# Kernel optimization log

Hardware: AMD Instinct MI355X
Metric: run time of the kernel (lower is better)

## Reference

```python
import jax, jax.numpy as jnp
import numpy as np

K = 16  # nsample for knn_point

def _bn(x, g, b):
    # inference-mode BatchNorm1d folded to per-channel affine (running stats 0/1)
    return x * g[None, :, None] + b[None, :, None]

def _knn(xyz, k):
    # xyz: [B,3,N] -> idx [B,N,k] of k nearest neighbors (squared L2)
    p = xyz.transpose(0, 2, 1)                                   # [B,N,3]
    sq = jnp.sum(p * p, axis=-1)                                 # [B,N]
    d = sq[:, :, None] + sq[:, None, :] - 2.0 * jnp.einsum('bnc,bmc->bnm', p, p)
    _, idx = jax.lax.top_k(-d, k)
    return idx

def _gather(hT, idx):
    # hT: [B,N,C], idx: [B,N,K] -> [B,N,K,C]
    return jax.vmap(lambda a, i: a[i])(hT, idx)

def setup_inputs():
    key = jax.random.key(0)
    ks = jax.random.split(key, 12)
    B, N, C = 16, 2048, 128
    def w(k, shape, fan):
        return jax.random.normal(k, shape, jnp.float32) * (1.0 / np.sqrt(fan))
    o = jnp.ones; z = jnp.zeros
    return {
        'points': jax.random.normal(ks[0], (B, 6, N), jnp.float32),
        'label': jax.random.uniform(ks[1], (B, 1, 16), jnp.float32),
        'We1': w(ks[2], (C, 6), 6), 'ge1': o(C), 'be1': z(C),
        'We2': w(ks[3], (C, C), C), 'ge2': o(C), 'be2': z(C),
        'W1': w(ks[4], (3, C, C), C), 'g1': o((3, C)), 'b1': z((3, C)),
        'W2': w(ks[5], (3, C, C), C), 'g2': o((3, C)), 'b2': z((3, C)),
        'Wf': w(ks[6], (1024, 3 * C), 3 * C), 'gf': o(1024), 'bf': z(1024),
        'Wl': w(ks[7], (64, 16), 16), 'gl': o(64), 'bl': z(64),
        'Wc1': w(ks[8], (512, 3136), 3136), 'bc1': z(512), 'gc1': o(512), 'bb1': z(512),
        'Wc2': w(ks[9], (256, 512), 512), 'bc2': z(256), 'gc2': o(256), 'bb2': z(256),
        'Wc3': w(ks[10], (50, 256), 256), 'bc3': z(50),
    }

def reference(points, label, We1, ge1, be1, We2, ge2, be2, W1, g1, b1, W2, g2, b2,
              Wf, gf, bf, Wl, gl, bl, Wc1, bc1, gc1, bb1, Wc2, bc2, gc2, bb2, Wc3, bc3):
    B, _, N = points.shape
    x = points[:, :6, :]
    xyz = x[:, :3, :]
    idx = _knn(xyz, K)                                            # [B,N,16]
    # input embedding: two conv1x1 + BN + ReLU
    h = jax.nn.relu(_bn(jnp.einsum('oc,bcn->bon', We1, x), ge1, be1))
    h = jax.nn.relu(_bn(jnp.einsum('oc,bcn->bon', We2, h), ge2, be2))
    xs = []
    for i in range(3):  # PVDSA_Res blocks (simplified: conv-BN-ReLU, kNN max-agg, conv-BN + residual)
        t = jax.nn.relu(_bn(jnp.einsum('oc,bcn->bon', W1[i], h), g1[i], b1[i]))
        nbr = _gather(t.transpose(0, 2, 1), idx)                  # [B,N,K,C]
        m = nbr.max(axis=2).transpose(0, 2, 1)                    # [B,C,N]
        h = jax.nn.relu(_bn(jnp.einsum('oc,bcn->bon', W2[i], m), g2[i], b2[i]) + h)
        xs.append(h)
    xcat = jnp.concatenate(xs, axis=1)                            # [B,384,N]
    xf = jax.nn.leaky_relu(_bn(jnp.einsum('oc,bcn->bon', Wf, xcat), gf, bf), 0.2)  # [B,1024,N]
    x_max = xf.max(axis=-1)                                       # [B,1024]
    x_avg = xf.mean(axis=-1)                                      # [B,1024]
    cls = jnp.broadcast_to(label.transpose(0, 2, 1), (B, 16, N))
    lab = jax.nn.leaky_relu(_bn(jnp.einsum('oc,bcn->bon', Wl, cls), gl, bl), 0.2)  # [B,64,N]
    glob = jnp.concatenate([
        jnp.broadcast_to(x_max[:, :, None], (B, 1024, N)),
        jnp.broadcast_to(x_avg[:, :, None], (B, 1024, N)),
        lab], axis=1)
    xa = jnp.concatenate([xf, glob], axis=1)                      # [B,3136,N]
    c = jax.nn.relu(_bn(jnp.einsum('oc,bcn->bon', Wc1, xa) + bc1[None, :, None], gc1, bb1))
    c = jax.nn.relu(_bn(jnp.einsum('oc,bcn->bon', Wc2, c) + bc2[None, :, None], gc2, bb2))
    out = jnp.einsum('oc,bcn->bon', Wc3, c) + bc3[None, :, None]  # [B,50,N]
    return out
```

## Files before the change

### kernel.cpp

```cpp
#include <hip/hip_runtime.h>
#include <cstdint>
#include <cstddef>

#define DEVINL __device__ __forceinline__

typedef float    f32x4 __attribute__((ext_vector_type(4)));
typedef _Float16 f16x8 __attribute__((ext_vector_type(8)));
typedef _Float16 f16x4 __attribute__((ext_vector_type(4)));

constexpr int BB = 16, NN = 2048, MM = 32768;

constexpr size_t OFF_WE1 = 0;
constexpr size_t OFF_WE2 = OFF_WE1 + 128 * 64 * 2;
constexpr size_t OFF_W1  = OFF_WE2 + 128 * 128 * 2;
constexpr size_t OFF_W2  = OFF_W1  + 3 * 128 * 128 * 2;
constexpr size_t OFF_WF  = OFF_W2  + 3 * 128 * 128 * 2;
constexpr size_t OFF_WC1 = OFF_WF  + 1024 * 384 * 2;
constexpr size_t OFF_WC2 = OFF_WC1 + 512 * 1024 * 2;
constexpr size_t OFF_WC3 = OFF_WC2 + 256 * 512 * 2;
constexpr size_t OFF_BC2 = OFF_WC3 + 128 * 256 * 2;
constexpr size_t OFF_BC3 = OFF_BC2 + 256 * 4;
constexpr size_t OFF_CVEC= OFF_BC3 + 128 * 4;
constexpr size_t OFF_PMAX= OFF_CVEC+ 16 * 512 * 4;
constexpr size_t OFF_PSUM= OFF_PMAX+ 16 * 16 * 1024 * 4;
constexpr size_t OFF_IDX = OFF_PSUM+ 16 * 16 * 1024 * 4;
constexpr size_t OFF_R1  = 8ull << 20;
constexpr size_t OFF_X0  = OFF_R1;
constexpr size_t OFF_HT  = OFF_R1 + (4ull  << 20);
constexpr size_t OFF_TT  = OFF_R1 + (12ull << 20);
constexpr size_t OFF_MT  = OFF_R1 + (20ull << 20);
constexpr size_t OFF_C1  = OFF_R1;
constexpr size_t OFF_XCAT= OFF_R1 + (32ull << 20);
constexpr size_t OFF_C2  = OFF_XCAT;
constexpr size_t OFF_XF  = OFF_XCAT + (24ull << 20);

__global__ __launch_bounds__(256) void fold_all_kernel(
    const float* We1, const float* ge1, const float* We2, const float* ge2,
    const float* W1,  const float* g1,  const float* W2,  const float* g2,
    const float* Wf,  const float* gf,  const float* Wc1, const float* gc1,
    const float* Wc2, const float* gc2, const float* Wc3,
    const float* gc2b, const float* bc2, const float* bb2, const float* bc3,
    const float* pts, char* ws)
{
    const int bid = blockIdx.x;
    const int tid = threadIdx.x;

    if (bid == 4704) {
        ((float*)(ws + OFF_BC2))[tid] = gc2b[tid] * bc2[tid] + bb2[tid];
        return;
    }
    if (bid == 4705) {
        if (tid < 128) ((float*)(ws + OFF_BC3))[tid] = (tid < 50) ? bc3[tid] : 0.f;
        return;
    }
    if (bid >= 4706) {
        int m = (bid - 4706) * 256 + tid;
        int b = m >> 11, n = m & 2047;
        const float* ps = pts + (size_t)b * 6 * 2048 + n;
        _Float16 tmp[64];
#pragma unroll
        for (int c = 0; c < 64; ++c) tmp[c] = (_Float16)0.f;
#pragma unroll
        for (int c = 0; c < 6; ++c) tmp[c] = (_Float16)ps[(size_t)c << 11];
        _Float16* dst = (_Float16*)(ws + OFF_X0) + (size_t)m * 64;
#pragma unroll
        for (int v = 0; v < 8; ++v) *(f16x8*)(dst + v * 8) = *(const f16x8*)(tmp + v * 8);
        return;
    }

    int id, base;
    if      (bid < 32)   { id = 0;  base = 0;    }
    else if (bid < 96)   { id = 1;  base = 32;   }
    else if (bid < 160)  { id = 2;  base = 96;   }
    else if (bid < 224)  { id = 3;  base = 160;  }
    else if (bid < 288)  { id = 4;  base = 224;  }
    else if (bid < 352)  { id = 5;  base = 288;  }
    else if (bid < 416)  { id = 6;  base = 352;  }
    else if (bid < 480)  { id = 7;  base = 416;  }
    else if (bid < 2016) { id = 8;  base = 480;  }
    else if (bid < 4064) { id = 9;  base = 2016; }
    else if (bid < 4576) { id = 10; base = 4064; }
    else                 { id = 11; base = 4576; }

    const float* src = nullptr; const float* g = nullptr; _Float16* dst = nullptr;
    int O = 0, K = 0, lds = 0, Kp = 0;
    switch (id) {
        case 0:  src = We1; g = ge1; O = 128; K = 6;    lds = 6;    Kp = 64;   dst = (_Float16*)(ws + OFF_WE1); break;
        case 1:  src = We2; g = ge2; O = 128; K = 128;  lds = 128;  Kp = 128;  dst = (_Float16*)(ws + OFF_WE2); break;
        case 2: case 3: case 4: {
            int i = id - 2;
            src = W1 + (size_t)i * 16384; g = g1 + i * 128; O = 128; K = 128; lds = 128; Kp = 128;
            dst = (_Float16*)(ws + OFF_W1) + (size_t)i * 16384; break; }
        case 5: case 6: case 7: {
            int i = id - 5;
            src = W2 + (size_t)i * 16384; g = g2 + i * 128; O = 128; K = 128; lds = 128; Kp = 128;
            dst = (_Float16*)(ws + OFF_W2) + (size_t)i * 16384; break; }
        case 8:  src = Wf;  g = gf;  O = 1024; K = 384;  lds = 384;  Kp = 384;  dst = (_Float16*)(ws + OFF_WF);  break;
        case 9:  src = Wc1; g = gc1; O = 512;  K = 1024; lds = 3136; Kp = 1024; dst = (_Float16*)(ws + OFF_WC1); break;
        case 10: src = Wc2; g = gc2; O = 256;  K = 512;  lds = 512;  Kp = 512;  dst = (_Float16*)(ws + OFF_WC2); break;
        default: src = Wc3; g = nullptr; O = 50; K = 256; lds = 256; Kp = 256;  dst = (_Float16*)(ws + OFF_WC3); break;
    }
    int e = (bid - base) * 256 + tid;
    int o = e / Kp, k = e - o * Kp;
    float v = 0.f;
    if (o < O && k < K) {
        v = src[(size_t)o * lds + k];
        if (g) v *= g[o];
    }
    dst[e] = (_Float16)v;
}

DEVINL float knn_dist(const float4 pq, const float4 pm) {
    float t = pq.x * pm.x;
    t = fmaf(pq.y, pm.y, t);
    t = fmaf(pq.z, pm.z, t);
    return fmaf(-2.f, t, pm.w);
}

#define KNN_DINS(X) do { \
    const float x_ = (X); \
    d15 = __builtin_amdgcn_fmed3f(x_, d14, d15); \
    d14 = __builtin_amdgcn_fmed3f(x_, d13, d14); \
    d13 = __builtin_amdgcn_fmed3f(x_, d12, d13); \
    d12 = __builtin_amdgcn_fmed3f(x_, d11, d12); \
    d11 = __builtin_amdgcn_fmed3f(x_, d10, d11); \
    d10 = __builtin_amdgcn_fmed3f(x_, d9,  d10); \
    d9  = __builtin_amdgcn_fmed3f(x_, d8,  d9);  \
    d8  = __builtin_amdgcn_fmed3f(x_, d7,  d8);  \
    d7  = __builtin_amdgcn_fmed3f(x_, d6,  d7);  \
    d6  = __builtin_amdgcn_fmed3f(x_, d5,  d6);  \
    d5  = __builtin_amdgcn_fmed3f(x_, d4,  d5);  \
    d4  = __builtin_amdgcn_fmed3f(x_, d3,  d4);  \
    d3  = __builtin_amdgcn_fmed3f(x_, d2,  d3);  \
    d2  = __builtin_amdgcn_fmed3f(x_, d1,  d2);  \
    d1  = __builtin_amdgcn_fmed3f(x_, d0,  d1);  \
    d0  = __builtin_amdgcn_fmed3f(x_, -3.4e38f, d0); \
} while (0)

#define KNN_CE(A, B) { const float lo_ = fminf(A, B), hi_ = fmaxf(A, B); A = lo_; B = hi_; }

#define KNN_MERGE(OFF) do { \
    const float n0  = __shfl_xor(d0,  OFF), n1  = __shfl_xor(d1,  OFF), \
                n2  = __shfl_xor(d2,  OFF), n3  = __shfl_xor(d3,  OFF), \
                n4  = __shfl_xor(d4,  OFF), n5  = __shfl_xor(d5,  OFF), \
                n6  = __shfl_xor(d6,  OFF), n7  = __shfl_xor(d7,  OFF), \
                n8  = __shfl_xor(d8,  OFF), n9  = __shfl_xor(d9,  OFF), \
                n10 = __shfl_xor(d10, OFF), n11 = __shfl_xor(d11, OFF), \
                n12 = __shfl_xor(d12, OFF), n13 = __shfl_xor(d13, OFF), \
                n14 = __shfl_xor(d14, OFF), n15 = __shfl_xor(d15, OFF); \
    d0  = fminf(d0,  n15); d1  = fminf(d1,  n14); d2  = fminf(d2,  n13); d3  = fminf(d3,  n12); \
    d4  = fminf(d4,  n11); d5  = fminf(d5,  n10); d6  = fminf(d6,  n9);  d7  = fminf(d7,  n8);  \
    d8  = fminf(d8,  n7);  d9  = fminf(d9,  n6);  d10 = fminf(d10, n5);  d11 = fminf(d11, n4);  \
    d12 = fminf(d12, n3);  d13 = fminf(d13, n2);  d14 = fminf(d14, n1);  d15 = fminf(d15, n0);  \
    KNN_CE(d0, d8)  KNN_CE(d1, d9)  KNN_CE(d2, d10) KNN_CE(d3, d11) \
    KNN_CE(d4, d12) KNN_CE(d5, d13) KNN_CE(d6, d14) KNN_CE(d7, d15) \
    KNN_CE(d0, d4)  KNN_CE(d1, d5)  KNN_CE(d2, d6)  KNN_CE(d3, d7)  \
    KNN_CE(d8, d12) KNN_CE(d9, d13) KNN_CE(d10,d14) KNN_CE(d11,d15) \
    KNN_CE(d0, d2)  KNN_CE(d1, d3)  KNN_CE(d4, d6)  KNN_CE(d5, d7)  \
    KNN_CE(d8, d10) KNN_CE(d9, d11) KNN_CE(d12,d14) KNN_CE(d13,d15) \
    KNN_CE(d0, d1)  KNN_CE(d2, d3)  KNN_CE(d4, d5)  KNN_CE(d6, d7)  \
    KNN_CE(d8, d9)  KNN_CE(d10,d11) KNN_CE(d12,d13) KNN_CE(d14,d15) \
// ... 89 lines not shown
    _Float16* B2s = SH + 28672;

    const int tid = threadIdx.x;
    const int lane = tid & 63, wave = tid >> 6;
    const int r = lane & 15, quad = lane >> 4;
    const int m_blk = blockIdx.x * 64;
    const int oh = (wave >> 1) * 64, mh = (wave & 1) * 32;

    const int srow  = wave * 8 + (lane >> 3);
    const int sslot = lane & 7;

#pragma unroll
    for (int t = 0; t < 4; ++t) {
        const int row = t * 32 + srow;
        const int gk = (sslot ^ (row & 7)) << 3;
        __builtin_amdgcn_global_load_lds(
            (const __attribute__((address_space(1))) unsigned int*)(W1e + (size_t)row * 64 + gk),
            (__attribute__((address_space(3))) unsigned int*)(A1s + t * 2048 + wave * 512),
            16, 0, 0);
    }
#pragma unroll
    for (int t = 0; t < 2; ++t) {
        const int row = t * 32 + srow;
        const int gk = (sslot ^ (row & 7)) << 3;
        __builtin_amdgcn_global_load_lds(
            (const __attribute__((address_space(1))) unsigned int*)(X + (size_t)(m_blk + row) * 64 + gk),
            (__attribute__((address_space(3))) unsigned int*)(B1s + t * 2048 + wave * 512),
            16, 0, 0);
    }
#pragma unroll
    for (int kt = 0; kt < 2; ++kt)
#pragma unroll
        for (int t = 0; t < 4; ++t) {
            const int row = t * 32 + srow;
            const int gk = kt * 64 + ((sslot ^ (row & 7)) << 3);
            __builtin_amdgcn_global_load_lds(
                (const __attribute__((address_space(1))) unsigned int*)(W2e + (size_t)row * 128 + gk),
                (__attribute__((address_space(3))) unsigned int*)(A2s + kt * 8192 + t * 2048 + wave * 512),
                16, 0, 0);
        }

    asm volatile("s_waitcnt vmcnt(8)" ::: "memory");
    __builtin_amdgcn_sched_barrier(0);
    __builtin_amdgcn_s_barrier();
    asm volatile("" ::: "memory");

    f32x4 acc1[4][2];
#pragma unroll
    for (int a = 0; a < 4; ++a)
#pragma unroll
        for (int c = 0; c < 2; ++c) acc1[a][c] = (f32x4){0.f, 0.f, 0.f, 0.f};
#pragma unroll
    for (int ks = 0; ks < 2; ++ks) {
        f16x8 af[4], bf[2];
#pragma unroll
        for (int oi = 0; oi < 4; ++oi) {
            const int row = oh + oi * 16 + r;
            const int slot = (ks * 4 + quad) ^ (row & 7);
            af[oi] = *(const f16x8*)(A1s + row * 64 + slot * 8);
        }
#pragma unroll
        for (int mi = 0; mi < 2; ++mi) {
            const int row = mh + mi * 16 + r;
            const int slot = (ks * 4 + quad) ^ (row & 7);
            bf[mi] = *(const f16x8*)(B1s + row * 64 + slot * 8);
        }
#pragma unroll
        for (int oi = 0; oi < 4; ++oi)
#pragma unroll
            for (int mi = 0; mi < 2; ++mi)
                acc1[oi][mi] = __builtin_amdgcn_mfma_f32_16x16x32_f16(af[oi], bf[mi], acc1[oi][mi], 0, 0, 0);
    }

#pragma unroll
    for (int oi = 0; oi < 4; ++oi) {
        const int ob = oh + oi * 16 + quad * 4;
        const f32x4 bv = *(const f32x4*)(b1v + ob);
        const int kt = ob >> 6, kk = ob & 63;
        const int chunk = kk >> 3, within = kk & 7;
#pragma unroll
        for (int mi = 0; mi < 2; ++mi) {
            const int row = mh + mi * 16 + r;
            f32x4 v = acc1[oi][mi] + bv;
            f16x4 ov;
#pragma unroll
            for (int j = 0; j < 4; ++j) { float x = v[j]; ov[j] = (_Float16)((x > 0.f) ? x : 0.f); }
            *(f16x4*)(B2s + kt * 4096 + row * 64 + ((chunk ^ (row & 7)) << 3) + within) = ov;
        }
    }
    __syncthreads();

    f32x4 acc2[4][2];
#pragma unroll
    for (int a = 0; a < 4; ++a)
#pragma unroll
        for (int c = 0; c < 2; ++c) acc2[a][c] = (f32x4){0.f, 0.f, 0.f, 0.f};
#pragma unroll
    for (int kt = 0; kt < 2; ++kt)
#pragma unroll
        for (int ks = 0; ks < 2; ++ks) {
            f16x8 af[4], bf[2];
#pragma unroll
            for (int oi = 0; oi < 4; ++oi) {
                const int row = oh + oi * 16 + r;
                const int slot = (ks * 4 + quad) ^ (row & 7);
                af[oi] = *(const f16x8*)(A2s + kt * 8192 + row * 64 + slot * 8);
            }
#pragma unroll
            for (int mi = 0; mi < 2; ++mi) {
                const int row = mh + mi * 16 + r;
                const int slot = (ks * 4 + quad) ^ (row & 7);
                bf[mi] = *(const f16x8*)(B2s + kt * 4096 + row * 64 + slot * 8);
            }
#pragma unroll
            for (int oi = 0; oi < 4; ++oi)
#pragma unroll
                for (int mi = 0; mi < 2; ++mi)
                    acc2[oi][mi] = __builtin_amdgcn_mfma_f32_16x16x32_f16(af[oi], bf[mi], acc2[oi][mi], 0, 0, 0);
        }
    __syncthreads();

    _Float16* OT = SH;
#pragma unroll
    for (int oi = 0; oi < 4; ++oi) {
        const int ol = oh + oi * 16 + quad * 4;
        const f32x4 bv = *(const f32x4*)(b2v + ol);
#pragma unroll
        for (int mi = 0; mi < 2; ++mi) {
            const int row = mh + mi * 16 + r;
            f32x4 v = acc2[oi][mi] + bv;
            f16x4 ov;
#pragma unroll
            for (int j = 0; j < 4; ++j) { float x = v[j]; ov[j] = (_Float16)((x > 0.f) ? x : 0.f); }
            const int s = ((ol >> 2) ^ (row & 31)) << 2;
            *(f16x4*)(OT + row * 128 + s) = ov;
        }
    }
    __syncthreads();
#pragma unroll
    for (int it2 = 0; it2 < 4; ++it2) {
        const int row = it2 * 16 + (tid >> 4);
        const int c = tid & 15;
        const int s0 = ((c * 2) ^ (row & 31)) << 2;
        const int s1 = ((c * 2 + 1) ^ (row & 31)) << 2;
        f16x4 a  = *(const f16x4*)(OT + row * 128 + s0);
        f16x4 b2 = *(const f16x4*)(OT + row * 128 + s1);
        f16x8 o8;
        o8[0] = a[0]; o8[1] = a[1]; o8[2] = a[2]; o8[3] = a[3];
        o8[4] = b2[0]; o8[5] = b2[1]; o8[6] = b2[2]; o8[7] = b2[3];
        *(f16x8*)(Y + (size_t)(m_blk + row) * 128 + c * 8) = o8;
    }
}

__global__ __launch_bounds__(256) void pair_kernel(
    const _Float16* __restrict__ Wa, const _Float16* __restrict__ Wb,
    const _Float16* __restrict__ X, const _Float16* __restrict__ Res,
    _Float16* __restrict__ Y1, _Float16* __restrict__ Y2,
    const float* __restrict__ ba, const float* __restrict__ bb,
    int ldR, int roff, int yoff1)
{
    __shared__ _Float16 SH[32768];
    _Float16* Aa  = SH;
    _Float16* Bx  = SH + 16384;
    _Float16* By1 = SH + 24576;
    _Float16* Ab  = SH;
    _Float16* OT2 = SH + 16384;

    const int tid = threadIdx.x;
    const int lane = tid & 63, wave = tid >> 6;
    const int r = lane & 15, quad = lane >> 4;
    const int m_blk = blockIdx.x * 64;
    const int oh = (wave >> 1) * 64, mh = (wave & 1) * 32;

    const int srow  = wave * 8 + (lane >> 3);
    const int sslot = lane & 7;

#pragma unroll
    for (int kt = 0; kt < 2; ++kt)
#pragma unroll
        for (int t = 0; t < 4; ++t) {
            const int row = t * 32 + srow;
            const int gk = kt * 64 + ((sslot ^ (row & 7)) << 3);
            __builtin_amdgcn_global_load_lds(
                (const __attribute__((address_space(1))) unsigned int*)(Wa + (size_t)row * 128 + gk),
                (__attribute__((address_space(3))) unsigned int*)(Aa + kt * 8192 + t * 2048 + wave * 512),
                16, 0, 0);
        }
#pragma unroll
    for (int kt = 0; kt < 2; ++kt)
#pragma unroll
        for (int t = 0; t < 2; ++t) {
            const int row = t * 32 + srow;
            const int gk = kt * 64 + ((sslot ^ (row & 7)) << 3);
            __builtin_amdgcn_global_load_lds(
                (const __attribute__((address_space(1))) unsigned int*)(X + (size_t)(m_blk + row) * 128 + gk),
                (__attribute__((address_space(3))) unsigned int*)(Bx + kt * 4096 + t * 2048 + wave * 512),
                16, 0, 0);
        }
    __syncthreads();

    f32x4 acc1[4][2];
#pragma unroll
    for (int a = 0; a < 4; ++a)
#pragma unroll
        for (int c = 0; c < 2; ++c) acc1[a][c] = (f32x4){0.f, 0.f, 0.f, 0.f};
#pragma unroll
    for (int kt = 0; kt < 2; ++kt)
#pragma unroll
        for (int ks = 0; ks < 2; ++ks) {
            f16x8 af[4], bf[2];
#pragma unroll
            for (int oi = 0; oi < 4; ++oi) {
                const int row = oh + oi * 16 + r;
                const int slot = (ks * 4 + quad) ^ (row & 7);
                af[oi] = *(const f16x8*)(Aa + kt * 8192 + row * 64 + slot * 8);
            }
#pragma unroll
            for (int mi = 0; mi < 2; ++mi) {
                const int row = mh + mi * 16 + r;
                const int slot = (ks * 4 + quad) ^ (row & 7);
                bf[mi] = *(const f16x8*)(Bx + kt * 4096 + row * 64 + slot * 8);
            }
#pragma unroll
            for (int oi = 0; oi < 4; ++oi)
#pragma unroll
                for (int mi = 0; mi < 2; ++mi)
                    acc1[oi][mi] = __builtin_amdgcn_mfma_f32_16x16x32_f16(af[oi], bf[mi], acc1[oi][mi], 0, 0, 0);
        }
    __syncthreads();

#pragma unroll
    for (int kt = 0; kt < 2; ++kt)
#pragma unroll
        for (int t = 0; t < 4; ++t) {
            const int row = t * 32 + srow;
            const int gk = kt * 64 + ((sslot ^ (row & 7)) << 3);
            __builtin_amdgcn_global_load_lds(
                (const __attribute__((address_space(1))) unsigned int*)(Wb + (size_t)row * 128 + gk),
                (__attribute__((address_space(3))) unsigned int*)(Ab + kt * 8192 + t * 2048 + wave * 512),
                16, 0, 0);
        }

#pragma unroll
    for (int oi = 0; oi < 4; ++oi) {
        const int ol = oh + oi * 16 + quad * 4;
        const f32x4 bv = *(const f32x4*)(ba + ol);
        const int kt = ol >> 6, kk = ol & 63;
        const int chunk = kk >> 3, within = kk & 7;
#pragma unroll
        for (int mi = 0; mi < 2; ++mi) {
            const int row = mh + mi * 16 + r;
            f32x4 v = acc1[oi][mi] + bv;
            f16x4 rr = *(const f16x4*)(Res + (size_t)(m_blk + row) * ldR + roff + ol);
#pragma unroll
            for (int j = 0; j < 4; ++j) v[j] += (float)rr[j];
            f16x4 ov;
#pragma unroll
            for (int j = 0; j < 4; ++j) { float x = v[j]; ov[j] = (_Float16)((x > 0.f) ? x : 0.f); }
            *(f16x4*)(By1 + kt * 4096 + row * 64 + ((chunk ^ (row & 7)) << 3) + within) = ov;
        }
    }
    __syncthreads();

#pragma unroll
    for (int it = 0; it < 4; ++it) {
        const int g = it * 256 + tid;
        const int row = g >> 4, c = g & 15;
        const int kt = c >> 3, cc = c & 7;
        f16x8 o8 = *(const f16x8*)(By1 + kt * 4096 + row * 64 + ((cc ^ (row & 7)) << 3));
        *(f16x8*)(Y1 + (size_t)(m_blk + row) * 384 + yoff1 + c * 8) = o8;
    }

    f32x4 acc2[4][2];
#pragma unroll
    for (int a = 0; a < 4; ++a)
#pragma unroll
        for (int c = 0; c < 2; ++c) acc2[a][c] = (f32x4){0.f, 0.f, 0.f, 0.f};
#pragma unroll
    for (int kt = 0; kt < 2; ++kt)
#pragma unroll
        for (int ks = 0; ks < 2; ++ks) {
            f16x8 af[4], bf[2];
#pragma unroll
            for (int oi = 0; oi < 4; ++oi) {
                const int row = oh + oi * 16 + r;
                const int slot = (ks * 4 + quad) ^ (row & 7);
                af[oi] = *(const f16x8*)(Ab + kt * 8192 + row * 64 + slot * 8);
            }
#pragma unroll
            for (int mi = 0; mi < 2; ++mi) {
                const int row = mh + mi * 16 + r;
                const int slot = (ks * 4 + quad) ^ (row & 7);
                bf[mi] = *(const f16x8*)(By1 + kt * 4096 + row * 64 + slot * 8);
            }
#pragma unroll
            for (int oi = 0; oi < 4; ++oi)
#pragma unroll
                for (int mi = 0; mi < 2; ++mi)
                    acc2[oi][mi] = __builtin_amdgcn_mfma_f32_16x16x32_f16(af[oi], bf[mi], acc2[oi][mi], 0, 0, 0);
        }

#pragma unroll
    for (int oi = 0; oi < 4; ++oi) {
        const int ol = oh + oi * 16 + quad * 4;
        const f32x4 bv = *(const f32x4*)(bb + ol);
#pragma unroll
        for (int mi = 0; mi < 2; ++mi) {
            const int row = mh + mi * 16 + r;
            f32x4 v = acc2[oi][mi] + bv;
            f16x4 ov;
#pragma unroll
            for (int j = 0; j < 4; ++j) { float x = v[j]; ov[j] = (_Float16)((x > 0.f) ? x : 0.f); }
            const int s = ((ol >> 2) ^ (row & 31)) << 2;
            *(f16x4*)(OT2 + row * 128 + s) = ov;
        }
    }
    __syncthreads();
#pragma unroll
    for (int it2 = 0; it2 < 4; ++it2) {
        const int row = it2 * 16 + (tid >> 4);
        const int c = tid & 15;
        const int s0 = ((c * 2) ^ (row & 31)) << 2;
        const int s1 = ((c * 2 + 1) ^ (row & 31)) << 2;
        f16x4 a  = *(const f16x4*)(OT2 + row * 128 + s0);
        f16x4 b2 = *(const f16x4*)(OT2 + row * 128 + s1);
        f16x8 o8;
        o8[0] = a[0]; o8[1] = a[1]; o8[2] = a[2]; o8[3] = a[3];
        o8[4] = b2[0]; o8[5] = b2[1]; o8[6] = b2[2]; o8[7] = b2[3];
        *(f16x8*)(Y2 + (size_t)(m_blk + row) * 128 + c * 8) = o8;
    }
}

__global__ __launch_bounds__(512, 2) void gemm256(
    const _Float16* __restrict__ W, const _Float16* __restrict__ X,
    _Float16* __restrict__ Y, const float* __restrict__ bias,
    int Kp, int ldX, int ldY, int Opad, int act, int biasPerBatch,
    float* __restrict__ pmax, float* __restrict__ psum)
{
    constexpr int ASZ = 256 * 64;
    __shared__ _Float16 SH[65536];
    const int tid  = threadIdx.x;
    const int lane = tid & 63, wave = tid >> 6;
    const int r = lane & 15, quad = lane >> 4;
    const int wo = wave & 3, wm = wave >> 2;
    const int m_blk = blockIdx.x * 256, o_blk = blockIdx.y * 256;
    const int nt = Kp >> 6;

    f32x4 acc[4][8];
#pragma unroll
    for (int a = 0; a < 4; ++a)
#pragma unroll
        for (int c = 0; c < 8; ++c) acc[a][c] = (f32x4){0.f, 0.f, 0.f, 0.f};

    const int srow  = wave * 8 + (lane >> 3);
    const int sslot = lane & 7;

    auto STAGE = [&](int bufi, int k0) {
        _Float16* As = SH + bufi * (2 * ASZ);
        _Float16* Bs = As + ASZ;
#pragma unroll
        for (int t = 0; t < 4; ++t) {
            const int rowA = t * 64 + srow;
            const int gk = k0 + ((sslot ^ (rowA & 7)) << 3);
            const _Float16* gA = W + (size_t)(o_blk + rowA) * Kp + gk;
            __builtin_amdgcn_global_load_lds(
                (const __attribute__((address_space(1))) unsigned int*)gA,
                (__attribute__((address_space(3))) unsigned int*)(As + t * 4096 + wave * 512),
                16, 0, 0);
        }
#pragma unroll
        for (int t = 0; t < 4; ++t) {
            const int rowB = t * 64 + srow;
            const int gk = k0 + ((sslot ^ (rowB & 7)) << 3);
            const _Float16* gB = X + (size_t)(m_blk + rowB) * ldX + gk;
            __builtin_amdgcn_global_load_lds(
                (const __attribute__((address_space(1))) unsigned int*)gB,
                (__attribute__((address_space(3))) unsigned int*)(Bs + t * 4096 + wave * 512),
                16, 0, 0);
        }
    };

    STAGE(0, 0);
    int cur = 0;
    for (int t = 0; t < nt; ++t) {
        if (t + 1 < nt) {
            STAGE(cur ^ 1, (t + 1) << 6);
            asm volatile("s_waitcnt vmcnt(8)" ::: "memory");
        } else {
            asm volatile("s_waitcnt vmcnt(0)" ::: "memory");
        }
        __builtin_amdgcn_sched_barrier(0);
        __builtin_amdgcn_s_barrier();
        asm volatile("" ::: "memory");

        const _Float16* As = SH + cur * (2 * ASZ);
        const _Float16* Bs = As + ASZ;
        __builtin_amdgcn_s_setprio(1);
#pragma unroll
        for (int ks = 0; ks < 2; ++ks) {
            f16x8 af[4], bf[8];
#pragma unroll
            for (int oi = 0; oi < 4; ++oi) {
                const int row = (wo << 6) + (oi << 4) + r;
                const int slot = (ks * 4 + quad) ^ (row & 7);
                af[oi] = *(const f16x8*)(As + row * 64 + slot * 8);
            }
#pragma unroll
            for (int mi = 0; mi < 8; ++mi) {
                const int row = (wm << 7) + (mi << 4) + r;
                const int slot = (ks * 4 + quad) ^ (row & 7);
                bf[mi] = *(const f16x8*)(Bs + row * 64 + slot * 8);
            }
#pragma unroll
            for (int oi = 0; oi < 4; ++oi)
#pragma unroll
                for (int mi = 0; mi < 8; ++mi)
                    acc[oi][mi] = __builtin_amdgcn_mfma_f32_16x16x32_f16(af[oi], bf[mi], acc[oi][mi], 0, 0, 0);
        }
        __builtin_amdgcn_s_setprio(0);
        asm volatile("" ::: "memory");
        __builtin_amdgcn_s_barrier();
        cur ^= 1;
    }
    __syncthreads();

    const int bb = biasPerBatch ? (m_blk >> 11) * Opad : 0;
    _Float16* OT = SH;
#pragma unroll
    for (int oi = 0; oi < 4; ++oi) {
        const int ol = (wo << 6) + (oi << 4) + (quad << 2);
        const f32x4 bv = *(const f32x4*)(bias + bb + o_blk + ol);
#pragma unroll
        for (int mi = 0; mi < 8; ++mi) {
            const int row = (wm << 7) + (mi << 4) + r;
            f32x4 v = acc[oi][mi] + bv;
            f16x4 ov;
#pragma unroll
            for (int j = 0; j < 4; ++j) {
                float x = v[j];
                if (act == 1)      x = (x > 0.f) ? x : 0.0f;
                else if (act == 2) x = (x > 0.f) ? x : 0.2f * x;
                ov[j] = (_Float16)x;
            }
            const int s = (ol >> 2) ^ (row & 31);
            *(f16x4*)(OT + row * 256 + s * 4) = ov;
        }
    }
    __syncthreads();
#pragma unroll
    for (int p2 = 0; p2 < 16; ++p2) {
        const int g = (p2 << 9) + tid;
        const int row = g >> 5, c = g & 31;
        const int s0 = ((c << 1)) ^ (row & 31);
        const int s1 = ((c << 1) | 1) ^ (row & 31);
        f16x4 a  = *(const f16x4*)(OT + row * 256 + s0 * 4);
        f16x4 b2 = *(const f16x4*)(OT + row * 256 + s1 * 4);
        f16x8 o8;
        o8[0] = a[0]; o8[1] = a[1]; o8[2] = a[2]; o8[3] = a[3];
        o8[4] = b2[0]; o8[5] = b2[1]; o8[6] = b2[2]; o8[7] = b2[3];
        *(f16x8*)(Y + (size_t)(m_blk + row) * ldY + o_blk + (c << 3)) = o8;
    }

    if (pmax) {
        const int cg = tid & 63, h8 = tid >> 6;
        float mx0 = -3.4e38f, mx1 = -3.4e38f, mx2 = -3.4e38f, mx3 = -3.4e38f;
        float sm0 = 0.f, sm1 = 0.f, sm2 = 0.f, sm3 = 0.f;
#pragma unroll
        for (int rr = 0; rr < 32; ++rr) {
            const int row = (h8 << 5) + rr;
            const f16x4 v = *(const f16x4*)(OT + row * 256 + ((cg ^ (row & 31)) << 2));
            const float x0 = (float)v[0], x1 = (float)v[1], x2 = (float)v[2], x3 = (float)v[3];
            mx0 = fmaxf(mx0, x0); sm0 += x0;
            mx1 = fmaxf(mx1, x1); sm1 += x1;
            mx2 = fmaxf(mx2, x2); sm2 += x2;
            mx3 = fmaxf(mx3, x3); sm3 += x3;
        }
        __syncthreads();
        float* PR = (float*)SH;
        float* pw = PR + (size_t)(((h8 << 8) + (cg << 2)) << 1);
        pw[0] = mx0; pw[1] = sm0; pw[2] = mx1; pw[3] = sm1;
        pw[4] = mx2; pw[5] = sm2; pw[6] = mx3; pw[7] = sm3;
        __syncthreads();
// ... 26 lines not shown

    const int tid  = threadIdx.x;
    const int lane = tid & 63, wave = tid >> 6;
    const int r = lane & 15, quad = lane >> 4;
    const int m_blk = blockIdx.x * TM, o_blk = blockIdx.y * 128;
    const int oh = (wave >> 1) * 64, mh = (wave & 1) * (TM / 2);

    f32x4 acc[4][MI];
#pragma unroll
    for (int a = 0; a < 4; ++a)
#pragma unroll
        for (int c = 0; c < MI; ++c) acc[a][c] = (f32x4){0.f, 0.f, 0.f, 0.f};

    const int srow  = wave * 8 + (lane >> 3);
    const int sslot = lane & 7;

    auto STAGE = [&](int bufi, int k0) {
        _Float16* As = SH + bufi * (ASZ + BSZ);
        _Float16* Bs = As + ASZ;
#pragma unroll
        for (int t = 0; t < 4; ++t) {
            const int rowA = t * 32 + srow;
            const int gk = k0 + ((sslot ^ (rowA & 7)) << 3);
            const _Float16* gA = W + (size_t)(o_blk + rowA) * Kp + gk;
            __builtin_amdgcn_global_load_lds(
                (const __attribute__((address_space(1))) unsigned int*)gA,
                (__attribute__((address_space(3))) unsigned int*)(As + t * 2048 + wave * 512),
                16, 0, 0);
        }
#pragma unroll
        for (int t = 0; t < TM / 32; ++t) {
            const int rowB = t * 32 + srow;
            const int gk = k0 + ((sslot ^ (rowB & 7)) << 3);
            const _Float16* gB = X + (size_t)(m_blk + rowB) * ldX + xoff + gk;
            __builtin_amdgcn_global_load_lds(
                (const __attribute__((address_space(1))) unsigned int*)gB,
                (__attribute__((address_space(3))) unsigned int*)(Bs + t * 2048 + wave * 512),
                16, 0, 0);
        }
    };

    const int nt = Kp >> 6;
    STAGE(0, 0);
    int cur = 0;
    for (int t = 0; t < nt; ++t) {
        if (t + 1 < nt) {
            STAGE(cur ^ 1, (t + 1) << 6);
            if constexpr (TM == 128) asm volatile("s_waitcnt vmcnt(8)" ::: "memory");
            else                     asm volatile("s_waitcnt vmcnt(6)" ::: "memory");
        } else {
            asm volatile("s_waitcnt vmcnt(0)" ::: "memory");
        }
        __builtin_amdgcn_sched_barrier(0);
        __builtin_amdgcn_s_barrier();
        asm volatile("" ::: "memory");

        const _Float16* As = SH + cur * (ASZ + BSZ);
        const _Float16* Bs = As + ASZ;
        __builtin_amdgcn_s_setprio(1);
#pragma unroll
        for (int ks = 0; ks < 2; ++ks) {
            f16x8 af[4], bf[MI];
#pragma unroll
            for (int oi = 0; oi < 4; ++oi) {
                const int row = oh + oi * 16 + r;
                const int slot = (ks * 4 + quad) ^ (row & 7);
                af[oi] = *(const f16x8*)(As + row * 64 + slot * 8);
            }
#pragma unroll
            for (int mi = 0; mi < MI; ++mi) {
                const int row = mh + mi * 16 + r;
                const int slot = (ks * 4 + quad) ^ (row & 7);
                bf[mi] = *(const f16x8*)(Bs + row * 64 + slot * 8);
            }
#pragma unroll
            for (int oi = 0; oi < 4; ++oi)
#pragma unroll
                for (int mi = 0; mi < MI; ++mi)
                    acc[oi][mi] = __builtin_amdgcn_mfma_f32_16x16x32_f16(af[oi], bf[mi], acc[oi][mi], 0, 0, 0);
        }
        __builtin_amdgcn_s_setprio(0);
        asm volatile("" ::: "memory");
        __builtin_amdgcn_s_barrier();
        cur ^= 1;
    }

    const int bb = biasPerBatch ? (m_blk >> 11) * Opad : 0;
    __syncthreads();

    if (Y32) {
#pragma unroll
        for (int oi = 0; oi < 4; ++oi) {
            const int og = o_blk + oh + oi * 16 + quad * 4;
            const f32x4 bv = *(const f32x4*)(bias + bb + og);
#pragma unroll
            for (int mi = 0; mi < MI; ++mi) {
                const int m = m_blk + mh + mi * 16 + r;
                const int bidx = m >> 11, n = m & 2047;
                f32x4 v = acc[oi][mi] + bv;
#pragma unroll
                for (int j = 0; j < 4; ++j) {
                    float x = v[j];
                    if (act == 1)      x = (x > 0.f) ? x : 0.0f;
                    else if (act == 2) x = (x > 0.f) ? x : 0.2f * x;
                    const int o = og + j;
                    if (o < Olimit)
                        Y32[((size_t)(bidx * 50 + o) << 11) + n] = x;
                }
            }
        }
        return;
    }

    _Float16* OT = SH;
#pragma unroll
    for (int oi = 0; oi < 4; ++oi) {
        const int ol = oh + oi * 16 + quad * 4;
        const f32x4 bv = *(const f32x4*)(bias + bb + o_blk + ol);
#pragma unroll
        for (int mi = 0; mi < MI; ++mi) {
            const int row = mh + mi * 16 + r;
            f32x4 v = acc[oi][mi] + bv;
            if (Res) {
                f16x4 rr = *(const f16x4*)(Res + (size_t)(m_blk + row) * ldR + roff + o_blk + ol);
#pragma unroll
                for (int j = 0; j < 4; ++j) v[j] += (float)rr[j];
            }
            f16x4 ov;
#pragma unroll
            for (int j = 0; j < 4; ++j) {
                float x = v[j];
                if (act == 1)      x = (x > 0.f) ? x : 0.0f;
                else if (act == 2) x = (x > 0.f) ? x : 0.2f * x;
                ov[j] = (_Float16)x;
            }
            const int s = ((ol >> 2) ^ (row & 31)) << 2;
            *(f16x4*)(OT + row * 128 + s) = ov;
        }
    }
    __syncthreads();
#pragma unroll
    for (int it2 = 0; it2 < TM / 16; ++it2) {
        const int row = it2 * 16 + (tid >> 4);
        const int c = tid & 15;
        const int s0 = ((c * 2) ^ (row & 31)) << 2;
        const int s1 = ((c * 2 + 1) ^ (row & 31)) << 2;
        f16x4 a = *(const f16x4*)(OT + row * 128 + s0);
        f16x4 b2 = *(const f16x4*)(OT + row * 128 + s1);
        f16x8 o8;
        o8[0] = a[0]; o8[1] = a[1]; o8[2] = a[2]; o8[3] = a[3];
        o8[4] = b2[0]; o8[5] = b2[1]; o8[6] = b2[2]; o8[7] = b2[3];
        *(f16x8*)(Y + (size_t)(m_blk + row) * ldY + yoff + o_blk + c * 8) = o8;
    }
}

typedef short s16x8 __attribute__((ext_vector_type(8)));
__global__ __launch_bounds__(256) void gather_max_kernel(
    const short* __restrict__ T, const int* __restrict__ idx, short* __restrict__ Mo)
{
    const int tid = threadIdx.x;
    const int p = blockIdx.x * 16 + (tid >> 4);
    const int l = tid & 15;
    const int b = p >> 11;
    const int* ip = idx + (size_t)p * 16;
    size_t row = (size_t)((b << 11) + ip[0]);
    s16x8 cur = *(const s16x8*)(T + row * 128 + l * 8);
    unsigned short best[8];
#pragma unroll
    for (int e = 0; e < 8; ++e) best[e] = (unsigned short)cur[e];
#pragma unroll
    for (int j = 1; j < 16; ++j) {
        row = (size_t)((b << 11) + ip[j]);
        s16x8 v = *(const s16x8*)(T + row * 128 + l * 8);
#pragma unroll
        for (int e = 0; e < 8; ++e) {
            unsigned short u = (unsigned short)v[e];
            if (u > best[e]) best[e] = u;
        }
    }
    s16x8 ov;
#pragma unroll
    for (int e = 0; e < 8; ++e) ov[e] = (short)best[e];
    *(s16x8*)(Mo + (size_t)p * 128 + l * 8) = ov;
}

__global__ __launch_bounds__(256) void cvec_kernel(
    const float* __restrict__ label, const float* __restrict__ Wl, const float* __restrict__ gl, const float* __restrict__ bl,
    const float* __restrict__ Wc1, const float* __restrict__ bc1, const float* __restrict__ gc1, const float* __restrict__ bb1,
    const float* __restrict__ pmax, const float* __restrict__ psum, float* __restrict__ cvec)
{
    __shared__ float v[2112];
    __shared__ float red[256];
    const int b = blockIdx.x, og = blockIdx.y, tid = threadIdx.x;
    for (int i = tid; i < 1024; i += 256) {
        float mx = -3.4e38f, sm = 0.f;
#pragma unroll
        for (int c = 0; c < 8; ++c) {
            mx = fmaxf(mx, pmax[((size_t)(b * 8 + c) << 10) + i]);
            sm += psum[((size_t)(b * 8 + c) << 10) + i];
        }
        v[i] = mx;
        v[1024 + i] = sm * (1.f / 2048.f);
    }
    if (tid < 64) {
        float s = 0.f;
        for (int i = 0; i < 16; ++i) s += Wl[tid * 16 + i] * label[b * 16 + i];
        s = gl[tid] * s + bl[tid];
        v[2048 + tid] = (s > 0.f) ? s : 0.2f * s;
    }
    __syncthreads();
    const int o = og * 64 + (tid >> 2), part = tid & 3;
    const float* wrow = Wc1 + (size_t)o * 3136 + 1024 + part * 528;
    float s = 0.f;
    for (int j = 0; j < 528; ++j) s += wrow[j] * v[part * 528 + j];
    red[tid] = s;
    __syncthreads();
    if (part == 0) {
        float tot = red[tid] + red[tid + 1] + red[tid + 2] + red[tid + 3];
        cvec[((size_t)b << 9) + o] = gc1[o] * (tot + bc1[o]) + bb1[o];
    }
}

extern "C" void kernel_launch(void* const* d_in, const int* in_sizes, int n_in,
                              void* d_out, int out_size, void* d_ws, size_t ws_size,
                              hipStream_t stream)
{
    (void)in_sizes; (void)n_in; (void)out_size; (void)ws_size;
    const float* points = (const float*)d_in[0];
    const float* label  = (const float*)d_in[1];
    const float* We1 = (const float*)d_in[2];
    const float* ge1 = (const float*)d_in[3];
    const float* be1 = (const float*)d_in[4];
    const float* We2 = (const float*)d_in[5];
    const float* ge2 = (const float*)d_in[6];
    const float* be2 = (const float*)d_in[7];
    const float* W1  = (const float*)d_in[8];
    const float* g1  = (const float*)d_in[9];
    const float* b1  = (const float*)d_in[10];
    const float* W2  = (const float*)d_in[11];
    const float* g2  = (const float*)d_in[12];
    const float* b2  = (const float*)d_in[13];
    const float* Wf  = (const float*)d_in[14];
    const float* gf  = (const float*)d_in[15];
    const float* bfv = (const float*)d_in[16];
    const float* Wl  = (const float*)d_in[17];
    const float* gl  = (const float*)d_in[18];
    const float* bl  = (const float*)d_in[19];
    const float* Wc1 = (const float*)d_in[20];
    const float* bc1 = (const float*)d_in[21];
    const float* gc1 = (const float*)d_in[22];
    const float* bb1 = (const float*)d_in[23];
    const float* Wc2 = (const float*)d_in[24];
    const float* bc2 = (const float*)d_in[25];
    const float* gc2 = (const float*)d_in[26];
    const float* bb2 = (const float*)d_in[27];
    const float* Wc3 = (const float*)d_in[28];
    const float* bc3 = (const float*)d_in[29];

    char* ws = (char*)d_ws;
    _Float16* hT  = (_Float16*)(ws + OFF_HT);
    _Float16* tT  = (_Float16*)(ws + OFF_TT);
    _Float16* mT  = (_Float16*)(ws + OFF_MT);
    _Float16* xct = (_Float16*)(ws + OFF_XCAT);
    _Float16* xf  = (_Float16*)(ws + OFF_XF);
    _Float16* c1  = (_Float16*)(ws + OFF_C1);
    _Float16* c2  = (_Float16*)(ws + OFF_C2);
    int*      idx = (int*)     (ws + OFF_IDX);
    _Float16* x0  = (_Float16*)(ws + OFF_X0);

    _Float16* wE1 = (_Float16*)(ws + OFF_WE1);
    _Float16* wE2 = (_Float16*)(ws + OFF_WE2);
    _Float16* w1f = (_Float16*)(ws + OFF_W1);
    _Float16* w2f = (_Float16*)(ws + OFF_W2);
    _Float16* wF  = (_Float16*)(ws + OFF_WF);
    _Float16* wC1 = (_Float16*)(ws + OFF_WC1);
    _Float16* wC2 = (_Float16*)(ws + OFF_WC2);
    _Float16* wC3 = (_Float16*)(ws + OFF_WC3);
    float* bC2 = (float*)(ws + OFF_BC2);
    float* bC3 = (float*)(ws + OFF_BC3);
    float* cv  = (float*)(ws + OFF_CVEC);
    float* pmx = (float*)(ws + OFF_PMAX);
    float* psm = (float*)(ws + OFF_PSUM);

    fold_all_kernel<<<dim3(4834), 256, 0, stream>>>(We1, ge1, We2, ge2, W1, g1, W2, g2,
                                                    Wf, gf, Wc1, gc1, Wc2, gc2, Wc3,
                                                    gc2, bc2, bb2, bc3, points, ws);
    knn_kernel<<<dim3(BB, NN / 32), 256, 0, stream>>>(points, idx);

    e12_kernel<<<dim3(512), 256, 0, stream>>>(wE1, wE2, x0, hT, be1, be2);

    gemm_tile<64><<<dim3(512, 1), 256, 0, stream>>>(w1f, hT, tT, nullptr, b1, nullptr,
                                                    128, 128, 0, 128, 0, 128, 1, 0, 0, 0, 128);
    gather_max_kernel<<<dim3(MM / 16), 256, 0, stream>>>((const short*)tT, idx, (short*)mT);

    pair_kernel<<<dim3(512), 256, 0, stream>>>(w2f, w1f + 16384, mT, hT, xct, tT,
                                               b2, b1 + 128, 128, 0, 0);
    gather_max_kernel<<<dim3(MM / 16), 256, 0, stream>>>((const short*)tT, idx, (short*)mT);

    pair_kernel<<<dim3(512), 256, 0, stream>>>(w2f + 16384, w1f + 2 * 16384, mT, xct, xct, tT,
                                               b2 + 128, b1 + 256, 384, 0, 128);
    gather_max_kernel<<<dim3(MM / 16), 256, 0, stream>>>((const short*)tT, idx, (short*)mT);

    gemm_tile<64><<<dim3(512, 1), 256, 0, stream>>>(w2f + 2 * 16384, mT, xct, nullptr, b2 + 256, xct,
                                                    128, 128, 0, 384, 256, 128, 1, 0, 384, 128, 128);

    gemm256<<<dim3(128, 4), 512, 0, stream>>>(wF, xct, xf, bfv, 384, 384, 1024, 1024, 2, 0, pmx, psm);

    cvec_kernel<<<dim3(BB, 8), 256, 0, stream>>>(label, Wl, gl, bl, Wc1, bc1, gc1, bb1, pmx, psm, cv);

    gemm256<<<dim3(128, 2), 512, 0, stream>>>(wC1, xf, c1, cv, 1024, 1024, 512, 512, 1, 1, nullptr, nullptr);

    gemm_tile<128><<<dim3(256, 2), 256, 0, stream>>>(wC2, c1, c2, nullptr, bC2, nullptr, 512, 512, 0, 256, 0, 256, 1, 0, 0, 0, 256);
    gemm_tile<128><<<dim3(256, 1), 256, 0, stream>>>(wC3, c2, nullptr, (float*)d_out, bC3, nullptr, 256, 256, 0, 0, 0, 128, 0, 0, 0, 0, 50);
}
```

Measured before the change: 368.9 us.

## Fuse neighbor gather-max into pair GEMM kernel and ping-pong T buffers

The separate gather_max kernel is folded into the pair kernel. Each block now gathers the 16 kNN rows and takes their max directly into LDS as the GEMM B operand, instead of writing mT to global memory and reading it back. The final block uses a template variant without the second GEMM, which replaces the last gemm_tile launch. This removes three kernel launches and an intermediate round trip. The cost is that the gather latency now sits on the GEMM block's critical path, since the old async LDS load is replaced by synchronous gathers, and T buffers ping-pong to avoid read/write races.

```diff
diff --git a/kernel.cpp b/kernel.cpp
--- a/kernel.cpp
+++ b/kernel.cpp
@@ -7,6 +7,7 @@
 typedef float    f32x4 __attribute__((ext_vector_type(4)));
 typedef _Float16 f16x8 __attribute__((ext_vector_type(8)));
 typedef _Float16 f16x4 __attribute__((ext_vector_type(4)));
+typedef short    s16x8 __attribute__((ext_vector_type(8)));
 
 constexpr int BB = 16, NN = 2048, MM = 32768;
 
@@ -402,16 +403,18 @@
     }
 }
 
-__global__ __launch_bounds__(256) void pair_kernel(
+template<bool HAS_G2>
+__global__ __launch_bounds__(256) void pairg_kernel(
     const _Float16* __restrict__ Wa, const _Float16* __restrict__ Wb,
-    const _Float16* __restrict__ X, const _Float16* __restrict__ Res,
+    const short* __restrict__ T, const int* __restrict__ idxp,
+    const _Float16* __restrict__ Res,
     _Float16* __restrict__ Y1, _Float16* __restrict__ Y2,
     const float* __restrict__ ba, const float* __restrict__ bb,
     int ldR, int roff, int yoff1)
 {
     __shared__ _Float16 SH[32768];
     _Float16* Aa  = SH;
-    _Float16* Bx  = SH + 16384;
+    _Float16* Bm  = SH + 16384;
     _Float16* By1 = SH + 24576;
     _Float16* Ab  = SH;
     _Float16* OT2 = SH + 16384;
@@ -436,17 +439,37 @@
                 (__attribute__((address_space(3))) unsigned int*)(Aa + kt * 8192 + t * 2048 + wave * 512),
                 16, 0, 0);
         }
-#pragma unroll
-    for (int kt = 0; kt < 2; ++kt)
-#pragma unroll
-        for (int t = 0; t < 2; ++t) {
-            const int row = t * 32 + srow;
-            const int gk = kt * 64 + ((sslot ^ (row & 7)) << 3);
-            __builtin_amdgcn_global_load_lds(
-                (const __attribute__((address_space(1))) unsigned int*)(X + (size_t)(m_blk + row) * 128 + gk),
-                (__attribute__((address_space(3))) unsigned int*)(Bx + kt * 4096 + t * 2048 + wave * 512),
-                16, 0, 0);
-        }
+
+    {
+        const int l = tid & 15;
+        const int kt = l >> 3, cc = l & 7;
+#pragma unroll
+        for (int it = 0; it < 4; ++it) {
+            const int row = it * 16 + (tid >> 4);
+            const int gm = m_blk + row;
+            const int b = gm >> 11;
+            const int* ip = idxp + (size_t)gm * 16;
+            size_t rr = (size_t)((b << 11) + ip[0]);
+            s16x8 cur = *(const s16x8*)(T + rr * 128 + l * 8);
+            unsigned short best[8];
+#pragma unroll
+            for (int e = 0; e < 8; ++e) best[e] = (unsigned short)cur[e];
+#pragma unroll
+            for (int j = 1; j < 16; ++j) {
+                rr = (size_t)((b << 11) + ip[j]);
+                s16x8 v = *(const s16x8*)(T + rr * 128 + l * 8);
+#pragma unroll
+                for (int e = 0; e < 8; ++e) {
+                    unsigned short u = (unsigned short)v[e];
+                    if (u > best[e]) best[e] = u;
+                }
+            }
+            s16x8 ov;
+#pragma unroll
+            for (int e = 0; e < 8; ++e) ov[e] = (short)best[e];
+            *(s16x8*)((short*)Bm + kt * 4096 + row * 64 + ((cc ^ (row & 7)) << 3)) = ov;
+        }
+    }
     __syncthreads();
 
     f32x4 acc1[4][2];
@@ -469,7 +492,7 @@
             for (int mi = 0; mi < 2; ++mi) {
                 const int row = mh + mi * 16 + r;
                 const int slot = (ks * 4 + quad) ^ (row & 7);
-                bf[mi] = *(const f16x8*)(Bx + kt * 4096 + row * 64 + slot * 8);
+                bf[mi] = *(const f16x8*)(Bm + kt * 4096 + row * 64 + slot * 8);
             }
 #pragma unroll
             for (int oi = 0; oi < 4; ++oi)
@@ -479,17 +502,19 @@
         }
     __syncthreads();
 
-#pragma unroll
-    for (int kt = 0; kt < 2; ++kt)
-#pragma unroll
-        for (int t = 0; t < 4; ++t) {
-            const int row = t * 32 + srow;
-            const int gk = kt * 64 + ((sslot ^ (row & 7)) << 3);
-            __builtin_amdgcn_global_load_lds(
-                (const __attribute__((address_space(1))) unsigned int*)(Wb + (size_t)row * 128 + gk),
-                (__attribute__((address_space(3))) unsigned int*)(Ab + kt * 8192 + t * 2048 + wave * 512),
-                16, 0, 0);
-        }
+    if constexpr (HAS_G2) {
+#pragma unroll
+        for (int kt = 0; kt < 2; ++kt)
+#pragma unroll
+            for (int t = 0; t < 4; ++t) {
+                const int row = t * 32 + srow;
+                const int gk = kt * 64 + ((sslot ^ (row & 7)) << 3);
+                __builtin_amdgcn_global_load_lds(
+                    (const __attribute__((address_space(1))) unsigned int*)(Wb + (size_t)row * 128 + gk),
+                    (__attribute__((address_space(3))) unsigned int*)(Ab + kt * 8192 + t * 2048 + wave * 512),
+                    16, 0, 0);
+            }
+    }
 
 #pragma unroll
     for (int oi = 0; oi < 4; ++oi) {
@@ -521,63 +546,65 @@
         *(f16x8*)(Y1 + (size_t)(m_blk + row) * 384 + yoff1 + c * 8) = o8;
     }
 
-    f32x4 acc2[4][2];
-#pragma unroll
-    for (int a = 0; a < 4; ++a)
-#pragma unroll
-        for (int c = 0; c < 2; ++c) acc2[a][c] = (f32x4){0.f, 0.f, 0.f, 0.f};
-#pragma unroll
-    for (int kt = 0; kt < 2; ++kt)
-#pragma unroll
-        for (int ks = 0; ks < 2; ++ks) {
-            f16x8 af[4], bf[2];
-#pragma unroll
-            for (int oi = 0; oi < 4; ++oi) {
-                const int row = oh + oi * 16 + r;
-                const int slot = (ks * 4 + quad) ^ (row & 7);
-                af[oi] = *(const f16x8*)(Ab + kt * 8192 + row * 64 + slot * 8);
-            }
+    if constexpr (HAS_G2) {
+        f32x4 acc2[4][2];
+#pragma unroll
+        for (int a = 0; a < 4; ++a)
+#pragma unroll
+            for (int c = 0; c < 2; ++c) acc2[a][c] = (f32x4){0.f, 0.f, 0.f, 0.f};
+#pragma unroll
+        for (int kt = 0; kt < 2; ++kt)
+#pragma unroll
+            for (int ks = 0; ks < 2; ++ks) {
+                f16x8 af[4], bf[2];
+#pragma unroll
+                for (int oi = 0; oi < 4; ++oi) {
+                    const int row = oh + oi * 16 + r;
+                    const int slot = (ks * 4 + quad) ^ (row & 7);
+                    af[oi] = *(const f16x8*)(Ab + kt * 8192 + row * 64 + slot * 8);
+                }
+#pragma unroll
+                for (int mi = 0; mi < 2; ++mi) {
+                    const int row = mh + mi * 16 + r;
+                    const int slot = (ks * 4 + quad) ^ (row & 7);
+                    bf[mi] = *(const f16x8*)(By1 + kt * 4096 + row * 64 + slot * 8);
+                }
+#pragma unroll
+                for (int oi = 0; oi < 4; ++oi)
+#pragma unroll
+                    for (int mi = 0; mi < 2; ++mi)
+                        acc2[oi][mi] = __builtin_amdgcn_mfma_f32_16x16x32_f16(af[oi], bf[mi], acc2[oi][mi], 0, 0, 0);
+            }
+
+#pragma unroll
+        for (int oi = 0; oi < 4; ++oi) {
+            const int ol = oh + oi * 16 + quad * 4;
+            const f32x4 bv = *(const f32x4*)(bb + ol);
 #pragma unroll
             for (int mi = 0; mi < 2; ++mi) {
                 const int row = mh + mi * 16 + r;
-                const int slot = (ks * 4 + quad) ^ (row & 7);
-                bf[mi] = *(const f16x8*)(By1 + kt * 4096 + row * 64 + slot * 8);
-            }
-#pragma unroll
-            for (int oi = 0; oi < 4; ++oi)
-#pragma unroll
-                for (int mi = 0; mi < 2; ++mi)
-                    acc2[oi][mi] = __builtin_amdgcn_mfma_f32_16x16x32_f16(af[oi], bf[mi], acc2[oi][mi], 0, 0, 0);
-        }
-
-#pragma unroll
-    for (int oi = 0; oi < 4; ++oi) {
-        const int ol = oh + oi * 16 + quad * 4;
-        const f32x4 bv = *(const f32x4*)(bb + ol);
-#pragma unroll
-        for (int mi = 0; mi < 2; ++mi) {
-            const int row = mh + mi * 16 + r;
-            f32x4 v = acc2[oi][mi] + bv;
-            f16x4 ov;
-#pragma unroll
-            for (int j = 0; j < 4; ++j) { float x = v[j]; ov[j] = (_Float16)((x > 0.f) ? x : 0.f); }
-            const int s = ((ol >> 2) ^ (row & 31)) << 2;
-            *(f16x4*)(OT2 + row * 128 + s) = ov;
-        }
-    }
-    __syncthreads();
-#pragma unroll
-    for (int it2 = 0; it2 < 4; ++it2) {
-        const int row = it2 * 16 + (tid >> 4);
-        const int c = tid & 15;
-        const int s0 = ((c * 2) ^ (row & 31)) << 2;
-        const int s1 = ((c * 2 + 1) ^ (row & 31)) << 2;
-        f16x4 a  = *(const f16x4*)(OT2 + row * 128 + s0);
-        f16x4 b2 = *(const f16x4*)(OT2 + row * 128 + s1);
-        f16x8 o8;
-        o8[0] = a[0]; o8[1] = a[1]; o8[2] = a[2]; o8[3] = a[3];
-        o8[4] = b2[0]; o8[5] = b2[1]; o8[6] = b2[2]; o8[7] = b2[3];
-        *(f16x8*)(Y2 + (size_t)(m_blk + row) * 128 + c * 8) = o8;
+                f32x4 v = acc2[oi][mi] + bv;
+                f16x4 ov;
+#pragma unroll
+                for (int j = 0; j < 4; ++j) { float x = v[j]; ov[j] = (_Float16)((x > 0.f) ? x : 0.f); }
+                const int s = ((ol >> 2) ^ (row & 31)) << 2;
+                *(f16x4*)(OT2 + row * 128 + s) = ov;
+            }
+        }
+        __syncthreads();
+#pragma unroll
+        for (int it2 = 0; it2 < 4; ++it2) {
+            const int row = it2 * 16 + (tid >> 4);
+            const int c = tid & 15;
+            const int s0 = ((c * 2) ^ (row & 31)) << 2;
+            const int s1 = ((c * 2 + 1) ^ (row & 31)) << 2;
+            f16x4 a  = *(const f16x4*)(OT2 + row * 128 + s0);
+            f16x4 b2 = *(const f16x4*)(OT2 + row * 128 + s1);
+            f16x8 o8;
+            o8[0] = a[0]; o8[1] = a[1]; o8[2] = a[2]; o8[3] = a[3];
+            o8[4] = b2[0]; o8[5] = b2[1]; o8[6] = b2[2]; o8[7] = b2[3];
+            *(f16x8*)(Y2 + (size_t)(m_blk + row) * 128 + c * 8) = o8;
+        }
     }
 }
 
@@ -910,36 +937,6 @@
         o8[4] = b2[0]; o8[5] = b2[1]; o8[6] = b2[2]; o8[7] = b2[3];
         *(f16x8*)(Y + (size_t)(m_blk + row) * ldY + yoff + o_blk + c * 8) = o8;
     }
-}
-
-typedef short s16x8 __attribute__((ext_vector_type(8)));
-__global__ __launch_bounds__(256) void gather_max_kernel(
-    const short* __restrict__ T, const int* __restrict__ idx, short* __restrict__ Mo)
-{
-    const int tid = threadIdx.x;
-    const int p = blockIdx.x * 16 + (tid >> 4);
-    const int l = tid & 15;
-    const int b = p >> 11;
-    const int* ip = idx + (size_t)p * 16;
-    size_t row = (size_t)((b << 11) + ip[0]);
-    s16x8 cur = *(const s16x8*)(T + row * 128 + l * 8);
-    unsigned short best[8];
-#pragma unroll
-    for (int e = 0; e < 8; ++e) best[e] = (unsigned short)cur[e];
-#pragma unroll
-    for (int j = 1; j < 16; ++j) {
-        row = (size_t)((b << 11) + ip[j]);
-        s16x8 v = *(const s16x8*)(T + row * 128 + l * 8);
-#pragma unroll
-        for (int e = 0; e < 8; ++e) {
-            unsigned short u = (unsigned short)v[e];
-            if (u > best[e]) best[e] = u;
-        }
-    }
-    s16x8 ov;
-#pragma unroll
-    for (int e = 0; e < 8; ++e) ov[e] = (short)best[e];
-    *(s16x8*)(Mo + (size_t)p * 128 + l * 8) = ov;
 }
 
 __global__ __launch_bounds__(256) void cvec_kernel(
@@ -1018,7 +1015,7 @@
     char* ws = (char*)d_ws;
     _Float16* hT  = (_Float16*)(ws + OFF_HT);
     _Float16* tT  = (_Float16*)(ws + OFF_TT);
-    _Float16* mT  = (_Float16*)(ws + OFF_MT);
+    _Float16* tT2 = (_Float16*)(ws + OFF_MT);
     _Float16* xct = (_Float16*)(ws + OFF_XCAT);
     _Float16* xf  = (_Float16*)(ws + OFF_XF);
     _Float16* c1  = (_Float16*)(ws + OFF_C1);
@@ -1049,18 +1046,15 @@
 
     gemm_tile<64><<<dim3(512, 1), 256, 0, stream>>>(w1f, hT, tT, nullptr, b1, nullptr,
                                                     128, 128, 0, 128, 0, 128, 1, 0, 0, 0, 128);
-    gather_max_kernel<<<dim3(MM / 16), 256, 0, stream>>>((const short*)tT, idx, (short*)mT);
-
-    pair_kernel<<<dim3(512), 256, 0, stream>>>(w2f, w1f + 16384, mT, hT, xct, tT,
-                                               b2, b1 + 128, 128, 0, 0);
-    gather_max_kernel<<<dim3(MM / 16), 256, 0, stream>>>((const short*)tT, idx, (short*)mT);
-
-    pair_kernel<<<dim3(512), 256, 0, stream>>>(w2f + 16384, w1f + 2 * 16384, mT, xct, xct, tT,
-                                               b2 + 128, b1 + 256, 384, 0, 128);
-    gather_max_kernel<<<dim3(MM / 16), 256, 0, stream>>>((const short*)tT, idx, (short*)mT);
-
-    gemm_tile<64><<<dim3(512, 1), 256, 0, stream>>>(w2f + 2 * 16384, mT, xct, nullptr, b2 + 256, xct,
-                                                    128, 128, 0, 384, 256, 128, 1, 0, 384, 128, 128);
+
+    pairg_kernel<true><<<dim3(512), 256, 0, stream>>>(w2f, w1f + 16384, (const short*)tT, idx, hT,
+                                                      xct, tT2, b2, b1 + 128, 128, 0, 0);
+
+    pairg_kernel<true><<<dim3(512), 256, 0, stream>>>(w2f + 16384, w1f + 2 * 16384, (const short*)tT2, idx, xct,
+                                                      xct, tT, b2 + 128, b1 + 256, 384, 0, 128);
+
+    pairg_kernel<false><<<dim3(512), 256, 0, stream>>>(w2f + 2 * 16384, nullptr, (const short*)tT, idx, xct,
+                                                       xct, nullptr, b2 + 256, nullptr, 384, 128, 256);
 
     gemm256<<<dim3(128, 4), 512, 0, stream>>>(wF, xct, xf, bfv, 384, 384, 1024, 1024, 2, 0, pmx, psm);
 
```

Result: no change. 366.2 us (-0.7%).
